# Optimization experiments

Hardware: AMD Instinct MI355X
Metric: run time of the kernel (lower is better)

## Reference

```python
import jax, jax.numpy as jnp
import numpy as np
from jax import lax

SEQ_SIZE = 4096
V = 4                               # vocab size
B = 256                             # batch
FILTER_SIZES = [4, 5, 6, 7, 8]
H = 10                              # lstm hidden
I = (len(FILTER_SIZES) + 1) * V     # lstm input size = 24


def setup_inputs() -> dict:
    key = jax.random.key(0)
    ks = jax.random.split(key, 9)
    inp = {"x": jax.random.normal(ks[0], (B, 1, V * SEQ_SIZE), dtype=jnp.float32)}
    for fs in FILTER_SIZES:
        # matches nn.init.constant_(conv.weight, 0.01)
        inp[f"w{fs}"] = jnp.full((1, 1, fs), 0.01, dtype=jnp.float32)
    s = 1.0 / float(np.sqrt(H))
    shapes = {"Wih": (4 * H, I), "Whh": (4 * H, H), "bih": (4 * H,), "bhh": (4 * H,)}
    k = 1
    for d in ("f", "r"):
        for nm, sh in shapes.items():
            inp[f"{nm}_{d}"] = jax.random.uniform(ks[k], sh, jnp.float32, -s, s)
            k += 1
    return inp


def _branch(x, w, fs):
    # x: (B,1,V*S); conv1d stride=V, VALID, no bias -> (B,1,L)
    conv = lax.conv_general_dilated(x, w, window_strides=(V,), padding="VALID",
                                    dimension_numbers=("NCH", "OIH", "NCH"))
    # winner_takes_all: (x + max_over_len)^2
    m = jnp.max(conv, axis=2, keepdims=True)
    v = ((conv + m) ** 2)[:, 0, :]                                  # (B,L)
    Bsz, L = v.shape
    # shape_convolutions2 == scatter-add of v[b,i] into out[b, V*i + j], j<fs
    idx = (V * jnp.arange(L)[:, None] + jnp.arange(fs)[None, :]).reshape(-1)
    contrib = jnp.broadcast_to(v[:, :, None], (Bsz, L, fs)).reshape(Bsz, -1)
    out = jnp.zeros((Bsz, V * SEQ_SIZE), v.dtype).at[:, idx].add(contrib)
    return out.reshape(Bsz, SEQ_SIZE, V)


def _lstm_dir(xs, Wih, Whh, bih, bhh, reverse):
    # xs: (S,B,I) -> hidden states (S,B,H), aligned with input positions
    Bsz = xs.shape[1]
    h0 = jnp.zeros((Bsz, H), xs.dtype)
    c0 = jnp.zeros((Bsz, H), xs.dtype)
    b = bih + bhh

    def step(carry, xt):
        h, c = carry
        g = xt @ Wih.T + h @ Whh.T + b          # (B,4H), torch gate order i,f,g,o
        i, f, gg, o = jnp.split(g, 4, axis=1)
        c = jax.nn.sigmoid(f) * c + jax.nn.sigmoid(i) * jnp.tanh(gg)
        h = jax.nn.sigmoid(o) * jnp.tanh(c)
        return (h, c), h

    _, hs = lax.scan(step, (h0, c0), xs, reverse=reverse)
    return hs


def _forward(x, ws, Wih_f, Whh_f, bih_f, bhh_f, Wih_r, Whh_r, bih_r, bhh_r):
    Bsz = x.shape[0]
    branches = [_branch(x, w, fs) for w, fs in zip(ws, FILTER_SIZES)]
    inp_r = x.reshape(Bsz, SEQ_SIZE, V)
    l_lstmin = jnp.concatenate(branches + [inp_r], axis=2)   # (B,S,24)
    xs = jnp.swapaxes(l_lstmin, 0, 1)                        # (S,B,24)
    hf = _lstm_dir(xs, Wih_f, Whh_f, bih_f, bhh_f, False)
    hr = _lstm_dir(xs, Wih_r, Whh_r, bih_r, bhh_r, True)
    h_sum = jnp.sum(hf, axis=2) + jnp.sum(hr, axis=2)        # (S,B)
    h_sum = h_sum.T                                          # (B,S)
    # l_in * repeated h_sum, reshaped and summed over vocab == inp_r * h_sum
    l_profile = jnp.sum(inp_r * h_sum[:, :, None], axis=2)   # (B,S)
    return jax.nn.sigmoid(jnp.sum(l_profile, axis=1, keepdims=True))  # (B,1)


def reference(x, w4, w5, w6, w7, w8, Wih_f, Whh_f, bih_f, bhh_f, Wih_r, Whh_r, bih_r, bhh_r):
    return _forward(x, [w4, w5, w6, w7, w8],
                    Wih_f, Whh_f, bih_f, bhh_f, Wih_r, Whh_r, bih_r, bhh_r)
```

## Files before the change

### kernel.cpp

```cpp
#include <hip/hip_runtime.h>

#define SEQ 4096
#define NBATCH 256

typedef float v2f __attribute__((ext_vector_type(2)));

__device__ __forceinline__ float sqf(float v) { return v * v; }
__device__ __forceinline__ float fexp2(float v) { return __builtin_amdgcn_exp2f(v); }
__device__ __forceinline__ float frcp(float v)  { return __builtin_amdgcn_rcpf(v); }

#define L2E 1.4426950408889634f

__device__ __forceinline__ unsigned fkey(float f) {
    const int b = __float_as_int(f);
    return (unsigned)(b ^ ((b >> 31) | 0x80000000));
}
__device__ __forceinline__ float fival(unsigned k) {
    const int b = (k & 0x80000000u) ? (int)(k ^ 0x80000000u) : (int)(~k);
    return __int_as_float(b);
}

__global__ void wprep_kernel(
    const float* __restrict__ Wih_f, const float* __restrict__ bih_f,
    const float* __restrict__ bhh_f,
    const float* __restrict__ Wih_r, const float* __restrict__ bih_r,
    const float* __restrict__ bhh_r,
    float* __restrict__ Wp, unsigned* __restrict__ MMu)
{
    const int t = threadIdx.x;
    for (int i = t; i < NBATCH * 5; i += 256) MMu[i] = 0u;
    if (t >= 80) return;
    const int d = t / 40, r = t % 40;
    const float* __restrict__ W  = (d ? Wih_r : Wih_f) + r * 24;
    const float* __restrict__ bi = d ? bih_r : bih_f;
    const float* __restrict__ bh = d ? bhh_r : bhh_f;
    const float sc = (r >= 20 && r < 30) ? (-2.f * L2E) : (-L2E);
    float o[13];
    o[0]  = W[0] + W[1] + W[2] + W[3];
    o[1]  = W[4] + W[5] + W[6] + W[7];
    o[2]  = W[4];
    o[3]  = W[8] + W[9] + W[10] + W[11];
    o[4]  = W[8] + W[9];
    o[5]  = W[12] + W[13] + W[14] + W[15];
    o[6]  = W[12] + W[13] + W[14];
    o[7]  = W[16] + W[17] + W[18] + W[19];
    o[8]  = W[20]; o[9] = W[21]; o[10] = W[22]; o[11] = W[23];
    o[12] = bi[r] + bh[r];
    float* __restrict__ out = Wp + (d * 40 + r) * 16;
#pragma unroll
    for (int k = 0; k < 13; ++k) out[k] = o[k] * sc;
    out[13] = 0.f; out[14] = 0.f; out[15] = 0.f;
}

__global__ __launch_bounds__(256) void max_kernel(
    const float* __restrict__ x,
    const float* __restrict__ w4p, const float* __restrict__ w5p,
    const float* __restrict__ w6p, const float* __restrict__ w7p,
    const float* __restrict__ w8p,
    unsigned* __restrict__ MMu)
{
    const int b    = blockIdx.x >> 2;
    const int quar = blockIdx.x & 3;
    const int tid  = threadIdx.x;
    const float* __restrict__ xr = x + (size_t)b * (4 * SEQ);

    float W4[4], W5[5], W6[6], W7[7], W8[8];
#pragma unroll
    for (int k = 0; k < 4; ++k) W4[k] = w4p[k];
#pragma unroll
    for (int k = 0; k < 5; ++k) W5[k] = w5p[k];
#pragma unroll
    for (int k = 0; k < 6; ++k) W6[k] = w6p[k];
#pragma unroll
    for (int k = 0; k < 7; ++k) W7[k] = w7p[k];
#pragma unroll
    for (int k = 0; k < 8; ++k) W8[k] = w8p[k];

    float m4 = -3.4e38f, m5 = -3.4e38f, m6 = -3.4e38f, m7 = -3.4e38f, m8 = -3.4e38f;
    for (int i = quar * (SEQ / 4) + tid; i < (quar + 1) * (SEQ / 4); i += 256) {
        const float4 t0 = *reinterpret_cast<const float4*>(xr + 4 * i);
        const float xa0 = t0.x, xa1 = t0.y, xa2 = t0.z, xa3 = t0.w;
        const float c4 = xa0 * W4[0] + xa1 * W4[1] + xa2 * W4[2] + xa3 * W4[3];
        m4 = fmaxf(m4, c4);
        if (i < SEQ - 1) {
            const float4 t1 = *reinterpret_cast<const float4*>(xr + 4 * i + 4);
            const float xa4 = t1.x, xa5 = t1.y, xa6 = t1.z, xa7 = t1.w;
            const float c5 = xa0*W5[0]+xa1*W5[1]+xa2*W5[2]+xa3*W5[3]+xa4*W5[4];
            const float c6 = xa0*W6[0]+xa1*W6[1]+xa2*W6[2]+xa3*W6[3]+xa4*W6[4]+xa5*W6[5];
            const float c7 = xa0*W7[0]+xa1*W7[1]+xa2*W7[2]+xa3*W7[3]+xa4*W7[4]+xa5*W7[5]+xa6*W7[6];
            const float c8 = xa0*W8[0]+xa1*W8[1]+xa2*W8[2]+xa3*W8[3]+xa4*W8[4]+xa5*W8[5]+xa6*W8[6]+xa7*W8[7];
            m5 = fmaxf(m5, c5); m6 = fmaxf(m6, c6);
            m7 = fmaxf(m7, c7); m8 = fmaxf(m8, c8);
        }
    }
#pragma unroll
    for (int off = 32; off; off >>= 1) {
        m4 = fmaxf(m4, __shfl_down(m4, off));
        m5 = fmaxf(m5, __shfl_down(m5, off));
        m6 = fmaxf(m6, __shfl_down(m6, off));
        m7 = fmaxf(m7, __shfl_down(m7, off));
        m8 = fmaxf(m8, __shfl_down(m8, off));
    }
    __shared__ float wr[4][5];
    if ((tid & 63) == 0) {
        const int w = tid >> 6;
        wr[w][0] = m4; wr[w][1] = m5; wr[w][2] = m6; wr[w][3] = m7; wr[w][4] = m8;
    }
    __syncthreads();
    if (tid < 5) {
        const float m = fmaxf(fmaxf(wr[0][tid], wr[1][tid]),
                              fmaxf(wr[2][tid], wr[3][tid]));
        atomicMax(&MMu[b * 5 + tid], fkey(m));
    }
}

__global__ __launch_bounds__(256) void scatter_kernel(
    const float* __restrict__ x,
    const float* __restrict__ w4p, const float* __restrict__ w5p,
    const float* __restrict__ w6p, const float* __restrict__ w7p,
    const float* __restrict__ w8p,
    const unsigned* __restrict__ MMu,
    float* __restrict__ lin)
{
    const int b    = blockIdx.x >> 2;
    const int quar = blockIdx.x & 3;
    const int tid  = threadIdx.x;
    const float* __restrict__ xr = x + (size_t)b * (4 * SEQ);

    float W4[4], W5[5], W6[6], W7[7], W8[8];
#pragma unroll
    for (int k = 0; k < 4; ++k) W4[k] = w4p[k];
#pragma unroll
    for (int k = 0; k < 5; ++k) W5[k] = w5p[k];
#pragma unroll
    for (int k = 0; k < 6; ++k) W6[k] = w6p[k];
#pragma unroll
    for (int k = 0; k < 7; ++k) W7[k] = w7p[k];
#pragma unroll
    for (int k = 0; k < 8; ++k) W8[k] = w8p[k];

    const float M4 = fival(MMu[b * 5 + 0]), M5 = fival(MMu[b * 5 + 1]),
                M6 = fival(MMu[b * 5 + 2]), M7 = fival(MMu[b * 5 + 3]),
                M8 = fival(MMu[b * 5 + 4]);

    for (int s = quar * (SEQ / 4) + tid; s < (quar + 1) * (SEQ / 4); s += 256) {
        float xw[12];
        if (s > 0) {
            const float4 t = *reinterpret_cast<const float4*>(xr + 4 * s - 4);
            xw[0] = t.x; xw[1] = t.y; xw[2] = t.z; xw[3] = t.w;
        } else { xw[0] = xw[1] = xw[2] = xw[3] = 0.f; }
        {
            const float4 t = *reinterpret_cast<const float4*>(xr + 4 * s);
            xw[4] = t.x; xw[5] = t.y; xw[6] = t.z; xw[7] = t.w;
        }
        if (s < SEQ - 1) {
            const float4 t = *reinterpret_cast<const float4*>(xr + 4 * s + 4);
            xw[8] = t.x; xw[9] = t.y; xw[10] = t.z; xw[11] = t.w;
        } else { xw[8] = xw[9] = xw[10] = xw[11] = 0.f; }

        float c4s = 0.f, c5s = 0.f, c6s = 0.f, c7s = 0.f, c8s = 0.f;
        float c5p = 0.f, c6p = 0.f, c7p = 0.f, c8p = 0.f;
#pragma unroll
        for (int t = 0; t < 4; ++t) c4s += xw[4 + t] * W4[t];
#pragma unroll
        for (int t = 0; t < 5; ++t) { c5s += xw[4 + t] * W5[t]; c5p += xw[t] * W5[t]; }
#pragma unroll
        for (int t = 0; t < 6; ++t) { c6s += xw[4 + t] * W6[t]; c6p += xw[t] * W6[t]; }
#pragma unroll
        for (int t = 0; t < 7; ++t) { c7s += xw[4 + t] * W7[t]; c7p += xw[t] * W7[t]; }
#pragma unroll
        for (int t = 0; t < 8; ++t) { c8s += xw[4 + t] * W8[t]; c8p += xw[t] * W8[t]; }

        const bool oks = (s < SEQ - 1);
        const bool okp = (s > 0);
        const float v4s = sqf(c4s + M4);
        const float v5s = oks ? sqf(c5s + M5) : 0.f;
        const float v6s = oks ? sqf(c6s + M6) : 0.f;
        const float v7s = oks ? sqf(c7s + M7) : 0.f;
        const float v8s = oks ? sqf(c8s + M8) : 0.f;
        const float v5p = okp ? sqf(c5p + M5) : 0.f;
        const float v6p = okp ? sqf(c6p + M6) : 0.f;
        const float v7p = okp ? sqf(c7p + M7) : 0.f;
        const float v8p = okp ? sqf(c8p + M8) : 0.f;

        const float xsum = (xw[4] + xw[5]) + (xw[6] + xw[7]);
        float4* op = reinterpret_cast<float4*>(lin + ((size_t)b * SEQ + s) * 16);
        op[0] = make_float4(v4s, v5s, v5p, v6s);
        op[1] = make_float4(v6p, v7s, v7p, v8s + v8p);
        op[2] = make_float4(xw[4], xw[5], xw[6], xw[7]);
        op[3] = make_float4(xsum, 0.f, 0.f, 0.f);
    }
}

__global__ __launch_bounds__(64, 2) void lstm_kernel(
    const float* __restrict__ lin,
    const float* __restrict__ Wp,
    const float* __restrict__ Whh_f,
    const float* __restrict__ Whh_r,
    float* __restrict__ P)
{
    const int bg   = blockIdx.x & 63;
    const int d    = (blockIdx.x >> 6) & 1;
    const int q    = blockIdx.x >> 7;
    const int b0   = bg * 4;
    const int lane = threadIdx.x;

    const int s0 = q * 256 - 128;
    const int nChunks = 24, warmChunks = 8;

    __shared__ float gbuf[16 * 4 * 44];
    __shared__ float xbuf[64];
    __shared__ float hb[64];

    const int c   = lane >> 4;
    const int jr  = lane & 15;
    const int jc  = (jr < 10) ? jr : 0;

    hb[lane] = 0.f;

    const float* __restrict__ Whh = d ? Whh_r : Whh_f;
    v2f wIF[10], wGO[10];
#pragma unroll
    for (int k = 0; k < 10; ++k) {
        wIF[k] = (v2f){Whh[jc * 10 + k]        * (-L2E),
                       Whh[(10 + jc) * 10 + k] * (-L2E)};
        wGO[k] = (v2f){Whh[(20 + jc) * 10 + k] * (-2.f * L2E),
                       Whh[(30 + jc) * 10 + k] * (-L2E)};
    }

    const float* __restrict__ Wd = Wp + d * 640;

    const int cc = lane & 3;
    const int r  = lane >> 2;
    const float* __restrict__ chbase = lin + (size_t)(b0 + cc) * SEQ * 16;

    auto rowp = [&](int cn) {
        int sp = s0 + cn * 16 + r;
        if (sp < 0) sp = 0;
        const int pos = d ? (SEQ - 1 - sp) : sp;
        return reinterpret_cast<const float4*>(chbase + (size_t)pos * 16);
    };

    float4 pA[4];
    {
        const float4* a = rowp(0);
        pA[0] = a[0]; pA[1] = a[1]; pA[2] = a[2]; pA[3] = a[3];
    }

    float cs = 0.f, accS = 0.f;

    auto step = [&](int i) {
        const float4 gp4 =
            *reinterpret_cast<const float4*>(&gbuf[(i * 4 + c) * 44 + jc * 4]);
        const float sx = xbuf[i * 4 + c];
        const float4 h03 = *reinterpret_cast<const float4*>(&hb[c * 16 + 0]);
        const float4 h47 = *reinterpret_cast<const float4*>(&hb[c * 16 + 4]);
        const float2 h89 = *reinterpret_cast<const float2*>(&hb[c * 16 + 8]);
        const float hj[10] = {h03.x, h03.y, h03.z, h03.w,
                              h47.x, h47.y, h47.z, h47.w, h89.x, h89.y};
        v2f eif0 = (v2f){gp4.x, gp4.y}, eif1 = (v2f){0.f, 0.f};
        v2f ego0 = (v2f){gp4.z, gp4.w}, ego1 = (v2f){0.f, 0.f};
#pragma unroll
        for (int k = 0; k < 10; k += 2) {
            const v2f h0 = (v2f){hj[k], hj[k]};
            const v2f h1 = (v2f){hj[k + 1], hj[k + 1]};
            eif0 += h0 * wIF[k]; eif1 += h1 * wIF[k + 1];
            ego0 += h0 * wGO[k]; ego1 += h1 * wGO[k + 1];
        }
        const v2f eif = eif0 + eif1, ego = ego0 + ego1;
        const float Ai = fexp2(eif.x);
        const float Fv = fexp2(eif.y);
        const float Bg = fexp2(fminf(ego.x, 80.f));
        const float Ov = fexp2(ego.y);
        const float sf = frcp(1.f + Fv);
        const float it = fmaf(Bg, 2.f * L2E, -2.f * L2E) *
                         frcp((1.f + Ai) * (1.f + Bg));
        cs = fmaf(sf, cs, it);
        const float Dv = fexp2(fminf(cs, 80.f));
        const float hv = (1.f - Dv) * frcp((1.f + Ov) * (1.f + Dv));
        hb[c * 16 + jr] = hv;
        accS = fmaf(sx, hv, accS);
    };

    for (int cn = 0; cn < nChunks; ++cn) {
        const float4 cA0 = pA[0], cA1 = pA[1], cA2 = pA[2], cA3 = pA[3];
        {
            const int nc = (cn + 1 < nChunks) ? cn + 1 : cn;
            const float4* a = rowp(nc);
            pA[0] = a[0]; pA[1] = a[1]; pA[2] = a[2]; pA[3] = a[3];
        }
        xbuf[r * 4 + cc] = cA3.x;
        float vv[12];
        vv[0] = cA0.x; vv[1] = cA0.y; vv[2]  = cA0.z; vv[3]  = cA0.w;
        vv[4] = cA1.x; vv[5] = cA1.y; vv[6]  = cA1.z; vv[7]  = cA1.w;
        vv[8] = cA2.x; vv[9] = cA2.y; vv[10] = cA2.z; vv[11] = cA2.w;
        const int wb = (r * 4 + cc) * 44;
#pragma unroll 2
        for (int j = 0; j < 10; ++j) {
            const float* __restrict__ R0 = Wd + j * 16;
            const float* __restrict__ R1 = Wd + (10 + j) * 16;
            const float* __restrict__ R2 = Wd + (20 + j) * 16;
            const float* __restrict__ R3 = Wd + (30 + j) * 16;
            v2f a01 = (v2f){R0[12], R1[12]}, b01 = (v2f){0.f, 0.f};
            v2f a23 = (v2f){R2[12], R3[12]}, b23 = (v2f){0.f, 0.f};
#pragma unroll
            for (int k = 0; k < 12; k += 2) {
                const v2f vk0 = (v2f){vv[k], vv[k]};
                const v2f vk1 = (v2f){vv[k + 1], vv[k + 1]};
                a01 += vk0 * (v2f){R0[k], R1[k]};
                b01 += vk1 * (v2f){R0[k + 1], R1[k + 1]};
                a23 += vk0 * (v2f){R2[k], R3[k]};
                b23 += vk1 * (v2f){R2[k + 1], R3[k + 1]};
            }
            const v2f s01 = a01 + b01, s23 = a23 + b23;
            *reinterpret_cast<float4*>(&gbuf[wb + j * 4]) =
                make_float4(s01.x, s01.y, s23.x, s23.y);
        }
        asm volatile("s_waitcnt lgkmcnt(0)" ::: "memory");
#pragma unroll 4
        for (int i = 0; i < 16; ++i) step(i);
        if (cn + 1 == warmChunks) {
            accS = 0.f;
            if (q == 0) {
                cs = 0.f;
                hb[lane] = 0.f;
            }
        }
    }

    float vA = (jr < 10) ? accS : 0.f;
#pragma unroll
    for (int off = 1; off <= 8; off <<= 1) vA += __shfl_down(vA, off);
    if (jr == 0) P[q * 512 + d * 256 + b0 + c] = vA;
}

__global__ __launch_bounds__(256) void final_kernel(const float* __restrict__ P,
                                                    float* __restrict__ out)
{
    const int b = threadIdx.x;
    float v = 0.f;
#pragma unroll
    for (int seg = 0; seg < 16; ++seg)
        v += P[seg * 512 + b] + P[seg * 512 + 256 + b];
    out[b] = frcp(1.f + fexp2(-v * L2E));
}

extern "C" void kernel_launch(void* const* d_in, const int* in_sizes, int n_in,
                              void* d_out, int out_size, void* d_ws, size_t ws_size,
                              hipStream_t stream)
{
    const float* x     = (const float*)d_in[0];
    const float* w4    = (const float*)d_in[1];
    const float* w5    = (const float*)d_in[2];
    const float* w6    = (const float*)d_in[3];
    const float* w7    = (const float*)d_in[4];
    const float* w8    = (const float*)d_in[5];
    const float* Wih_f = (const float*)d_in[6];
    const float* Whh_f = (const float*)d_in[7];
    const float* bih_f = (const float*)d_in[8];
    const float* bhh_f = (const float*)d_in[9];
    const float* Wih_r = (const float*)d_in[10];
    const float* Whh_r = (const float*)d_in[11];
    const float* bih_r = (const float*)d_in[12];
    const float* bhh_r = (const float*)d_in[13];

    float*    lin = (float*)d_ws;
    float*    P   = lin + (size_t)NBATCH * SEQ * 16;
    unsigned* MMu = (unsigned*)(P + 8192);
    float*    Wpp = (float*)(MMu + 1280);

    wprep_kernel<<<1, 256, 0, stream>>>(Wih_f, bih_f, bhh_f,
                                        Wih_r, bih_r, bhh_r, Wpp, MMu);
    max_kernel<<<4 * NBATCH, 256, 0, stream>>>(x, w4, w5, w6, w7, w8, MMu);
    scatter_kernel<<<4 * NBATCH, 256, 0, stream>>>(x, w4, w5, w6, w7, w8, MMu, lin);
    lstm_kernel<<<2048, 64, 0, stream>>>(lin, Wpp, Whh_f, Whh_r, P);
    final_kernel<<<1, NBATCH, 0, stream>>>(P, (float*)d_out);
}
```

Before: 269.6 us.

## Fuse LSTM input projection into recurrent step with register-resident weights

The per-chunk precompute of input-gate pre-activations into a shared gate buffer (ten rows by four gates per timestep) is removed. Each lane now keeps its own unit's 13x4 input weights in registers, re-laid out by the prep kernel as unit-major with the gate innermost, and computes the input projection inside every recurrent step from raw features staged in shared memory. This drops the bulk gate-buffer write, its shared footprint, and the redundant weight loads from global memory. In exchange it adds 24 packed FMAs plus extra shared-memory reads to the serial per-timestep dependency chain, and raises register pressure.

Result: faster. 254.7 us (-5.5%).

```diff
diff --git a/kernel.cpp b/kernel.cpp
--- a/kernel.cpp
+++ b/kernel.cpp
@@ -25,16 +25,17 @@
     const float* __restrict__ bhh_f,
     const float* __restrict__ Wih_r, const float* __restrict__ bih_r,
     const float* __restrict__ bhh_r,
-    float* __restrict__ Wp, unsigned* __restrict__ MMu)
+    float* __restrict__ Wq, unsigned* __restrict__ MMu)
 {
     const int t = threadIdx.x;
     for (int i = t; i < NBATCH * 5; i += 256) MMu[i] = 0u;
     if (t >= 80) return;
     const int d = t / 40, r = t % 40;
+    const int gate = r / 10, unit = r % 10;
     const float* __restrict__ W  = (d ? Wih_r : Wih_f) + r * 24;
     const float* __restrict__ bi = d ? bih_r : bih_f;
     const float* __restrict__ bh = d ? bhh_r : bhh_f;
-    const float sc = (r >= 20 && r < 30) ? (-2.f * L2E) : (-L2E);
+    const float sc = (gate == 2) ? (-2.f * L2E) : (-L2E);
     float o[13];
     o[0]  = W[0] + W[1] + W[2] + W[3];
     o[1]  = W[4] + W[5] + W[6] + W[7];
@@ -46,10 +47,9 @@
     o[7]  = W[16] + W[17] + W[18] + W[19];
     o[8]  = W[20]; o[9] = W[21]; o[10] = W[22]; o[11] = W[23];
     o[12] = bi[r] + bh[r];
-    float* __restrict__ out = Wp + (d * 40 + r) * 16;
-#pragma unroll
-    for (int k = 0; k < 13; ++k) out[k] = o[k] * sc;
-    out[13] = 0.f; out[14] = 0.f; out[15] = 0.f;
+#pragma unroll
+    for (int k = 0; k < 13; ++k)
+        Wq[(((d * 10) + unit) * 13 + k) * 4 + gate] = o[k] * sc;
 }
 
 __global__ __launch_bounds__(256) void max_kernel(
@@ -194,7 +194,7 @@
 
 __global__ __launch_bounds__(64, 2) void lstm_kernel(
     const float* __restrict__ lin,
-    const float* __restrict__ Wp,
+    const float* __restrict__ Wq,
     const float* __restrict__ Whh_f,
     const float* __restrict__ Whh_r,
     float* __restrict__ P)
@@ -208,8 +208,7 @@
     const int s0 = q * 256 - 128;
     const int nChunks = 24, warmChunks = 8;
 
-    __shared__ float gbuf[16 * 4 * 44];
-    __shared__ float xbuf[64];
+    __shared__ float vbuf[1024];
     __shared__ float hb[64];
 
     const int c   = lane >> 4;
@@ -218,6 +217,17 @@
 
     hb[lane] = 0.f;
 
+    v2f wINif[13], wINgo[13];
+    {
+        const float4* __restrict__ Wqp =
+            reinterpret_cast<const float4*>(Wq) + (d * 10 + jc) * 13;
+#pragma unroll
+        for (int k = 0; k < 13; ++k) {
+            const float4 w = Wqp[k];
+            wINif[k] = (v2f){w.x, w.y};
+            wINgo[k] = (v2f){w.z, w.w};
+        }
+    }
     const float* __restrict__ Whh = d ? Whh_r : Whh_f;
     v2f wIF[10], wGO[10];
 #pragma unroll
@@ -228,38 +238,52 @@
                        Whh[(30 + jc) * 10 + k] * (-L2E)};
     }
 
-    const float* __restrict__ Wd = Wp + d * 640;
-
-    const int cc = lane & 3;
-    const int r  = lane >> 2;
-    const float* __restrict__ chbase = lin + (size_t)(b0 + cc) * SEQ * 16;
-
-    auto rowp = [&](int cn) {
-        int sp = s0 + cn * 16 + r;
+    const int lc = lane & 3;
+    const int lr = lane >> 2;
+    const float* __restrict__ chbase = lin + (size_t)(b0 + lc) * SEQ * 16;
+
+    auto srcp = [&](int cn) {
+        int sp = s0 + cn * 16 + lr;
         if (sp < 0) sp = 0;
         const int pos = d ? (SEQ - 1 - sp) : sp;
         return reinterpret_cast<const float4*>(chbase + (size_t)pos * 16);
     };
 
-    float4 pA[4];
+    float4 pR0, pR1, pR2, pR3;
     {
-        const float4* a = rowp(0);
-        pA[0] = a[0]; pA[1] = a[1]; pA[2] = a[2]; pA[3] = a[3];
+        const float4* a = srcp(0);
+        pR0 = a[0]; pR1 = a[1]; pR2 = a[2]; pR3 = a[3];
     }
 
     float cs = 0.f, accS = 0.f;
 
     auto step = [&](int i) {
-        const float4 gp4 =
-            *reinterpret_cast<const float4*>(&gbuf[(i * 4 + c) * 44 + jc * 4]);
-        const float sx = xbuf[i * 4 + c];
+        const int ro = (i * 4 + c) * 4;
+        const float4 q0 = *reinterpret_cast<const float4*>(&vbuf[ro]);
+        const float4 q1 = *reinterpret_cast<const float4*>(&vbuf[256 + ro]);
+        const float4 q2 = *reinterpret_cast<const float4*>(&vbuf[512 + ro]);
+        const float  sx = vbuf[768 + ro];
+        const float vv[12] = {q0.x, q0.y, q0.z, q0.w,
+                              q1.x, q1.y, q1.z, q1.w,
+                              q2.x, q2.y, q2.z, q2.w};
+        v2f eI0 = wINif[12], eI1 = (v2f){0.f, 0.f};
+        v2f eG0 = wINgo[12], eG1 = (v2f){0.f, 0.f};
+#pragma unroll
+        for (int k = 0; k < 12; k += 2) {
+            const v2f v0 = (v2f){vv[k], vv[k]};
+            const v2f v1 = (v2f){vv[k + 1], vv[k + 1]};
+            eI0 += v0 * wINif[k]; eI1 += v1 * wINif[k + 1];
+            eG0 += v0 * wINgo[k]; eG1 += v1 * wINgo[k + 1];
+        }
+        const v2f sIF = eI0 + eI1;
+        const v2f sGO = eG0 + eG1;
         const float4 h03 = *reinterpret_cast<const float4*>(&hb[c * 16 + 0]);
         const float4 h47 = *reinterpret_cast<const float4*>(&hb[c * 16 + 4]);
         const float2 h89 = *reinterpret_cast<const float2*>(&hb[c * 16 + 8]);
         const float hj[10] = {h03.x, h03.y, h03.z, h03.w,
                               h47.x, h47.y, h47.z, h47.w, h89.x, h89.y};
-        v2f eif0 = (v2f){gp4.x, gp4.y}, eif1 = (v2f){0.f, 0.f};
-        v2f ego0 = (v2f){gp4.z, gp4.w}, ego1 = (v2f){0.f, 0.f};
+        v2f eif0 = sIF, eif1 = (v2f){0.f, 0.f};
+        v2f ego0 = sGO, ego1 = (v2f){0.f, 0.f};
 #pragma unroll
         for (int k = 0; k < 10; k += 2) {
             const v2f h0 = (v2f){hj[k], hj[k]};
@@ -283,40 +307,16 @@
     };
 
     for (int cn = 0; cn < nChunks; ++cn) {
-        const float4 cA0 = pA[0], cA1 = pA[1], cA2 = pA[2], cA3 = pA[3];
+        *reinterpret_cast<float4*>(&vbuf[lane * 4])       = pR0;
+        *reinterpret_cast<float4*>(&vbuf[256 + lane * 4]) = pR1;
+        *reinterpret_cast<float4*>(&vbuf[512 + lane * 4]) = pR2;
+        *reinterpret_cast<float4*>(&vbuf[768 + lane * 4]) = pR3;
+        asm volatile("s_waitcnt lgkmcnt(0)" ::: "memory");
         {
             const int nc = (cn + 1 < nChunks) ? cn + 1 : cn;
-            const float4* a = rowp(nc);
-            pA[0] = a[0]; pA[1] = a[1]; pA[2] = a[2]; pA[3] = a[3];
-        }
-        xbuf[r * 4 + cc] = cA3.x;
-        float vv[12];
-        vv[0] = cA0.x; vv[1] = cA0.y; vv[2]  = cA0.z; vv[3]  = cA0.w;
-        vv[4] = cA1.x; vv[5] = cA1.y; vv[6]  = cA1.z; vv[7]  = cA1.w;
-        vv[8] = cA2.x; vv[9] = cA2.y; vv[10] = cA2.z; vv[11] = cA2.w;
-        const int wb = (r * 4 + cc) * 44;
-#pragma unroll 2
-        for (int j = 0; j < 10; ++j) {
-            const float* __restrict__ R0 = Wd + j * 16;
-            const float* __restrict__ R1 = Wd + (10 + j) * 16;
-            const float* __restrict__ R2 = Wd + (20 + j) * 16;
-            const float* __restrict__ R3 = Wd + (30 + j) * 16;
-            v2f a01 = (v2f){R0[12], R1[12]}, b01 = (v2f){0.f, 0.f};
-            v2f a23 = (v2f){R2[12], R3[12]}, b23 = (v2f){0.f, 0.f};
-#pragma unroll
-            for (int k = 0; k < 12; k += 2) {
-                const v2f vk0 = (v2f){vv[k], vv[k]};
-                const v2f vk1 = (v2f){vv[k + 1], vv[k + 1]};
-                a01 += vk0 * (v2f){R0[k], R1[k]};
-                b01 += vk1 * (v2f){R0[k + 1], R1[k + 1]};
-                a23 += vk0 * (v2f){R2[k], R3[k]};
-                b23 += vk1 * (v2f){R2[k + 1], R3[k + 1]};
-            }
-            const v2f s01 = a01 + b01, s23 = a23 + b23;
-            *reinterpret_cast<float4*>(&gbuf[wb + j * 4]) =
-                make_float4(s01.x, s01.y, s23.x, s23.y);
-        }
-        asm volatile("s_waitcnt lgkmcnt(0)" ::: "memory");
+            const float4* a = srcp(nc);
+            pR0 = a[0]; pR1 = a[1]; pR2 = a[2]; pR3 = a[3];
+        }
 #pragma unroll 4
         for (int i = 0; i < 16; ++i) step(i);
         if (cn + 1 == warmChunks) {
@@ -367,12 +367,12 @@
     float*    lin = (float*)d_ws;
     float*    P   = lin + (size_t)NBATCH * SEQ * 16;
     unsigned* MMu = (unsigned*)(P + 8192);
-    float*    Wpp = (float*)(MMu + 1280);
+    float*    Wqp = (float*)(MMu + 1280);
 
     wprep_kernel<<<1, 256, 0, stream>>>(Wih_f, bih_f, bhh_f,
-                                        Wih_r, bih_r, bhh_r, Wpp, MMu);
+                                        Wih_r, bih_r, bhh_r, Wqp, MMu);
     max_kernel<<<4 * NBATCH, 256, 0, stream>>>(x, w4, w5, w6, w7, w8, MMu);
     scatter_kernel<<<4 * NBATCH, 256, 0, stream>>>(x, w4, w5, w6, w7, w8, MMu, lin);
-    lstm_kernel<<<2048, 64, 0, stream>>>(lin, Wpp, Whh_f, Whh_r, P);
+    lstm_kernel<<<2048, 64, 0, stream>>>(lin, Wqp, Whh_f, Whh_r, P);
     final_kernel<<<1, NBATCH, 0, stream>>>(P, (float*)d_out);
 }
```
